# Optimization experiments

Hardware: AMD Instinct MI355X
Metric: run time of the kernel (lower is better)

## Reference

```python
import jax, jax.numpy as jnp
import numpy as np
from jax import lax

NUM_TAGS = 19
IN_DIM = 202
HID = 100
B, T = 256, 512


def setup_inputs() -> dict:
    key = jax.random.key(0)
    ks = jax.random.split(key, 16)
    u = lambda k, shape, s: jax.random.uniform(k, shape, jnp.float32, -s, s)
    sh = 1.0 / np.sqrt(HID)
    sl = 1.0 / np.sqrt(2 * HID)
    x = jax.random.normal(ks[0], (B, T, IN_DIM), jnp.float32)
    lengths = jax.random.randint(ks[1], (B,), 1, T + 1)
    raw_tags = jax.random.randint(ks[2], (B, T), 0, NUM_TAGS)
    y = jnp.where(jnp.arange(T)[None, :] < lengths[:, None], raw_tags, -1)
    return dict(
        x=x, y=y,
        w_ih_f=u(ks[3], (HID, IN_DIM), sh), w_hh_f=u(ks[4], (HID, HID), sh),
        b_ih_f=u(ks[5], (HID,), sh), b_hh_f=u(ks[6], (HID,), sh),
        w_ih_b=u(ks[7], (HID, IN_DIM), sh), w_hh_b=u(ks[8], (HID, HID), sh),
        b_ih_b=u(ks[9], (HID,), sh), b_hh_b=u(ks[10], (HID,), sh),
        w_lin=u(ks[11], (NUM_TAGS, 2 * HID), sl), b_lin=u(ks[12], (NUM_TAGS,), sl),
        start_trans=u(ks[13], (NUM_TAGS,), 0.1),
        end_trans=u(ks[14], (NUM_TAGS,), 0.1),
        trans=u(ks[15], (NUM_TAGS, NUM_TAGS), 0.1),
    )


def _rnn_dir(x, w_ih, w_hh, b_ih, b_hh, reverse):
    # torch nn.RNN (tanh) scans over axis 0 of x (batch_first=False semantics)
    def step(h, xt):
        h = jnp.tanh(xt @ w_ih.T + b_ih + h @ w_hh.T + b_hh)
        return h, h
    h0 = jnp.zeros((x.shape[1], w_hh.shape[0]), x.dtype)
    _, hs = lax.scan(step, h0, x, reverse=reverse)
    return hs  # (S, N, HID)


def _emissions(x, w_ih_f, w_hh_f, b_ih_f, b_hh_f, w_ih_b, w_hh_b, b_ih_b, b_hh_b, w_lin, b_lin):
    hf = _rnn_dir(x, w_ih_f, w_hh_f, b_ih_f, b_hh_f, False)
    hb = _rnn_dir(x, w_ih_b, w_hh_b, b_ih_b, b_hh_b, True)
    h = jnp.concatenate([hf, hb], axis=-1)  # (B, T, 200)
    return jax.nn.softmax(h @ w_lin.T + b_lin, axis=2)  # (B, T, 19)


def _crf_llh(em, tags, mask, start, end, trans):
    # emissions (B,T,K) batch_first -> transpose to (T,B,*) for the scans
    em_t = jnp.swapaxes(em, 0, 1)
    tg = jnp.where(jnp.swapaxes(mask, 0, 1), jnp.swapaxes(tags, 0, 1), 0)
    mk = jnp.swapaxes(mask, 0, 1)
    mf = mk.astype(em.dtype)
    # numerator: gold path score
    s0 = start[tg[0]] + jnp.take_along_axis(em_t[0], tg[0][:, None], 1)[:, 0]
    def num_step(carry, inp):
        s, prev = carry
        e, t, m, mb = inp
        emit = jnp.take_along_axis(e, t[:, None], 1)[:, 0]
        s = s + (trans[prev, t] + emit) * m
        prev = jnp.where(mb, t, prev)  # track tag at last valid position
        return (s, prev), None
    (num, last), _ = lax.scan(num_step, (s0, tg[0]), (em_t[1:], tg[1:], mf[1:], mk[1:]))
    num = num + end[last]
    # denominator: masked forward algorithm
    def z_step(s, inp):
        e, mb = inp
        nxt = jax.nn.logsumexp(s[:, :, None] + trans[None] + e[:, None, :], axis=1)
        return jnp.where(mb[:, None], nxt, s), None
    z, _ = lax.scan(z_step, start + em_t[0], (em_t[1:], mk[1:]))
    logz = jax.nn.logsumexp(z + end, axis=1)
    return num - logz  # (B,) log-likelihood per sequence


def _viterbi(em, mask, start, end, trans):
    em_t = jnp.swapaxes(em, 0, 1)
    mk = jnp.swapaxes(mask, 0, 1)
    def fstep(s, inp):
        e, mb = inp
        cand = s[:, :, None] + trans[None] + e[:, None, :]  # (B,K,K)
        nxt = jnp.where(mb[:, None], jnp.max(cand, axis=1), s)
        return nxt, jnp.argmax(cand, axis=1)
    score, hist = lax.scan(fstep, start + em_t[0], (em_t[1:], mk[1:]))  # hist (T-1,B,K)
    best_last = jnp.argmax(score + end, axis=1)  # tag at each sequence end
    def bstep(tag, inp):
        h, mb = inp
        prev = jnp.take_along_axis(h, tag[:, None], 1)[:, 0]
        tag = jnp.where(mb, prev, tag)
        return tag, tag
    _, tags_bt = lax.scan(bstep, best_last, (hist, mk[1:]), reverse=True)  # (T-1,B), position order
    tags = jnp.concatenate([tags_bt, best_last[None]], axis=0)  # (T,B)
    tags = jnp.swapaxes(tags, 0, 1)
    return jnp.where(mask, tags, -1)  # pad with -1 like the torch pad_sequence


def reference(x, y, w_ih_f, w_hh_f, b_ih_f, b_hh_f, w_ih_b, w_hh_b, b_ih_b, b_hh_b, w_lin, b_lin, start_trans, end_trans, trans):
    mask = y != -1
    em = _emissions(x, w_ih_f, w_hh_f, b_ih_f, b_hh_f, w_ih_b, w_hh_b, b_ih_b, b_hh_b, w_lin, b_lin)
    loss = -jnp.sum(_crf_llh(em, y, mask, start_trans, end_trans, trans))  # reduction='sum'
    label = _viterbi(em, mask, start_trans, end_trans, trans)
    return loss, label
```

## Files before the change

kernel.cpp:

```cpp
#include <hip/hip_runtime.h>
#include <hip/hip_bf16.h>

#define B_ 256
#define T_ 512
#define IN_ 202
#define HID_ 100
#define K_ 19

typedef __attribute__((ext_vector_type(8))) short short8v;
typedef __attribute__((ext_vector_type(4))) float f32x4;

__device__ __forceinline__ float rl_f(float v, int l) {
  return __int_as_float(__builtin_amdgcn_readlane(__float_as_int(v), l));
}

__global__ __launch_bounds__(256, 1) void k_wprep(
    const float* __restrict__ wf, const float* __restrict__ wb,
    unsigned short* __restrict__ w3) {
  int idx = blockIdx.x * 256 + threadIdx.x;
  if (idx >= 224 * 224) return;
  int c = idx / 224, k = idx - (idx / 224) * 224;
  float v = 0.f;
  if (k < IN_) {
    if (c < 100) v = wf[c * IN_ + k];
    else if (c < 200) v = wb[(c - 100) * IN_ + k];
  }
  unsigned u0 = __float_as_uint(v) & 0xffff0000u;
  float r1 = v - __uint_as_float(u0);
  unsigned u1 = __float_as_uint(r1) & 0xffff0000u;
  float r2 = r1 - __uint_as_float(u1);
  w3[idx] = (unsigned short)(u0 >> 16);
  w3[50176 + idx] = (unsigned short)(u1 >> 16);
  w3[100352 + idx] = (unsigned short)(__float_as_uint(r2) >> 16);
}

__global__ __launch_bounds__(256, 2) void k_ih(
    const float* __restrict__ x, const unsigned short* __restrict__ w3,
    const float* __restrict__ bif, const float* __restrict__ bhf,
    const float* __restrict__ bib, const float* __restrict__ bhb,
    float* __restrict__ pre) {
  __shared__ float xs[256 * 36];
  __shared__ float bsum[224];
  int tid = threadIdx.x;
  int wv = tid >> 6, l = tid & 63;
  long row0 = (long)blockIdx.x * 256;
  for (int u = tid; u < 224; u += 256) {
    float bv = 0.f;
    if (u < 100) bv = bif[u] + bhf[u];
    else if (u < 200) bv = bib[u - 100] + bhb[u - 100];
    bsum[u] = bv;
  }
  int lr = l & 15;
  int kq = l >> 4;
  for (int g = 0; g < 2; g++) {
    f32x4 acc[4][7];
#pragma unroll
    for (int m = 0; m < 4; m++)
#pragma unroll
      for (int n = 0; n < 7; n++) acc[m][n] = (f32x4){0.f, 0.f, 0.f, 0.f};
    for (int ck = 0; ck < 7; ck++) {
      int k0 = ck * 32;
      __syncthreads();
#pragma unroll
      for (int i = 0; i < 16; i++) {
        int u = tid + i * 256;
        int r = u >> 4, kp = u & 15;
        int gk = k0 + 2 * kp;
        float2 v = make_float2(0.f, 0.f);
        if (gk < IN_) v = *(const float2*)(x + (row0 + r) * IN_ + gk);
        *(float2*)(&xs[r * 36 + 2 * kp]) = v;
      }
      __syncthreads();
      short8v A0[4], A1[4], A2[4];
#pragma unroll
      for (int m = 0; m < 4; m++) {
        const float* ap = &xs[(wv * 64 + m * 16 + lr) * 36 + kq * 8];
        float4 fa = *(const float4*)(ap);
        float4 fb = *(const float4*)(ap + 4);
        float f[8] = {fa.x, fa.y, fa.z, fa.w, fb.x, fb.y, fb.z, fb.w};
#pragma unroll
        for (int j = 0; j < 8; j++) {
          unsigned u0 = __float_as_uint(f[j]) & 0xffff0000u;
          float r1 = f[j] - __uint_as_float(u0);
          unsigned u1 = __float_as_uint(r1) & 0xffff0000u;
          float r2 = r1 - __uint_as_float(u1);
          A0[m][j] = (short)(u0 >> 16);
          A1[m][j] = (short)(u1 >> 16);
          A2[m][j] = (short)(__float_as_uint(r2) >> 16);
        }
      }
#pragma unroll
      for (int n = 0; n < 7; n++) {
        int col = (g * 7 + n) * 16 + lr;
        const unsigned short* bp = w3 + (long)col * 224 + k0 + kq * 8;
        short8v B0 = *(const short8v*)(bp);
        short8v B1 = *(const short8v*)(bp + 50176);
        short8v B2 = *(const short8v*)(bp + 100352);
#pragma unroll
        for (int m = 0; m < 4; m++) {
          f32x4 c = acc[m][n];
          c = __builtin_amdgcn_mfma_f32_16x16x32_bf16(A0[m], B0, c, 0, 0, 0);
          c = __builtin_amdgcn_mfma_f32_16x16x32_bf16(A0[m], B1, c, 0, 0, 0);
          c = __builtin_amdgcn_mfma_f32_16x16x32_bf16(A1[m], B0, c, 0, 0, 0);
          c = __builtin_amdgcn_mfma_f32_16x16x32_bf16(A0[m], B2, c, 0, 0, 0);
          c = __builtin_amdgcn_mfma_f32_16x16x32_bf16(A2[m], B0, c, 0, 0, 0);
          c = __builtin_amdgcn_mfma_f32_16x16x32_bf16(A1[m], B1, c, 0, 0, 0);
          c = __builtin_amdgcn_mfma_f32_16x16x32_bf16(A1[m], B2, c, 0, 0, 0);
          c = __builtin_amdgcn_mfma_f32_16x16x32_bf16(A2[m], B1, c, 0, 0, 0);
          acc[m][n] = c;
        }
      }
    }
#pragma unroll
    for (int m = 0; m < 4; m++) {
      long rbase = row0 + wv * 64 + m * 16 + kq * 4;
#pragma unroll
      for (int n = 0; n < 7; n++) {
        int col = (g * 7 + n) * 16 + lr;
        if (col < 200) {
          float bv = bsum[col];
#pragma unroll
          for (int r = 0; r < 4; r++)
            pre[(rbase + r) * 200 + col] = acc[m][n][r] + bv;
        }
      }
    }
  }
}

template <int KO, int KN, bool OW>
__device__ __forceinline__ void rnn_loop(
    float* __restrict__ p, long step, int row, bool owns,
    const float* __restrict__ w, float (*hb)[104], float* __restrict__ ps) {
  float wr[KN];
#pragma unroll
  for (int i = 0; i < KN / 4; i++) {
    float4 w4 = *(const float4*)(w + row * HID_ + KO + 4 * i);
    wr[4 * i + 0] = w4.x; wr[4 * i + 1] = w4.y;
    wr[4 * i + 2] = w4.z; wr[4 * i + 3] = w4.w;
  }
  float a = 0.f;
  if (OW) a = p[row];
  for (int s = 0; s < B_; s++) {
    int cur = s & 1;
    float a_next = 0.f;
    if (OW && s < B_ - 1) a_next = p[step + row];
    float ac0 = OW ? a : 0.f, ac1 = 0.f, ac2 = 0.f, ac3 = 0.f;
#pragma unroll
    for (int i = 0; i < KN / 4; i++) {
      float4 h4 = *(const float4*)(&hb[cur][KO + 4 * i]);
      ac0 = fmaf(h4.x, wr[4 * i + 0], ac0);
      ac1 = fmaf(h4.y, wr[4 * i + 1], ac1);
      ac2 = fmaf(h4.z, wr[4 * i + 2], ac2);
      ac3 = fmaf(h4.w, wr[4 * i + 3], ac3);
    }
    float partial = (ac0 + ac1) + (ac2 + ac3);
    if (!OW && owns) ps[row] = partial;
    __syncthreads();
    if (OW) {
      float hnew = tanhf(partial + ps[row]);
      if (owns) {
        hb[cur ^ 1][row] = hnew;
        p[row] = hnew;
      }
    }
    p += step;
    a = a_next;
    __syncthreads();
  }
}

__global__ __launch_bounds__(256, 4) void k_rnn(
    float* __restrict__ pre,
    const float* __restrict__ whf, const float* __restrict__ whb) {
  __shared__ float hb[2][104];
  __shared__ float ps[104];
  int bid = blockIdx.x;
  int dir = bid >> 9;
  int t = bid & 511;
  const float* w = dir ? whb : whf;
  int tid = threadIdx.x;
  int wv = tid >> 6, lane = tid & 63;
  int grp = wv >> 1;
  int khalf = wv & 1;
  int row = grp ? (64 + (lane < 36 ? lane : 35)) : lane;
  bool owns = grp ? (lane < 36) : true;
  long step = dir ? -(long)(T_ * 200) : (long)(T_ * 200);
  float* p = pre + ((long)(dir ? (B_ - 1) : 0) * T_ + t) * 200 + dir * 100;
  if (tid < 104) hb[0][tid] = 0.f;
  __syncthreads();
  if (khalf == 0) rnn_loop<0, 52, true >(p, step, row, owns, w, hb, ps);
  else            rnn_loop<52, 48, false>(p, step, row, owns, w, hb, ps);
}

__global__ __launch_bounds__(256, 4) void k_lin(
    const float* __restrict__ h, const float* __restrict__ wlin,
    const float* __restrict__ blin, float* __restrict__ em) {
  int tid = threadIdx.x;
  long r0 = ((long)blockIdx.x * 256 + tid) * 2;
  const float* h0 = h + r0 * 200;
  float acc0[K_], acc1[K_];
#pragma unroll
  for (int c = 0; c < K_; c++) { float bb = blin[c]; acc0[c] = bb; acc1[c] = bb; }
  for (int kk = 0; kk < 50; kk++) {
    float4 a = *(const float4*)(h0 + 4 * kk);
    float4 b = *(const float4*)(h0 + 200 + 4 * kk);
#pragma unroll
    for (int c = 0; c < K_; c++) {
      float4 wv = *(const float4*)(wlin + c * 200 + 4 * kk);
      acc0[c] += a.x * wv.x + a.y * wv.y + a.z * wv.z + a.w * wv.w;
      acc1[c] += b.x * wv.x + b.y * wv.y + b.z * wv.z + b.w * wv.w;
    }
  }
  float mx0 = acc0[0], mx1 = acc1[0];
#pragma unroll
  for (int c = 1; c < K_; c++) { mx0 = fmaxf(mx0, acc0[c]); mx1 = fmaxf(mx1, acc1[c]); }
  float s0 = 0.f, s1 = 0.f;
#pragma unroll
  for (int c = 0; c < K_; c++) {
    acc0[c] = __expf(acc0[c] - mx0); s0 += acc0[c];
    acc1[c] = __expf(acc1[c] - mx1); s1 += acc1[c];
  }
  float i0 = 1.f / s0, i1 = 1.f / s1;
  float* e0 = em + r0 * K_;
#pragma unroll
  for (int c = 0; c < K_; c++) { e0[c] = acc0[c] * i0; e0[K_ + c] = acc1[c] * i1; }
}

__global__ __launch_bounds__(128, 1) void k_crf(
    const float* __restrict__ em, const int* __restrict__ y,
    const float* __restrict__ st_g, const float* __restrict__ en_g,
    const float* __restrict__ tr_g,
    float* __restrict__ part, int* __restrict__ cnt,
    float* __restrict__ out) {
  __shared__ __align__(16) float es[T_ * K_];
  __shared__ int ys[T_];
  __shared__ float tr[K_ * K_];
  __shared__ float st[K_], en[K_];
  __shared__ unsigned char hl[511 * K_ + 13];
  __shared__ float lab[T_];
  int b = blockIdx.x;
  int tid = threadIdx.x;
  const float4* eb4 = (const float4*)(em + (long)b * T_ * K_);
  for (int u = tid; u < T_ * K_ / 4; u += 128) ((float4*)es)[u] = eb4[u];
  for (int u = tid; u < T_; u += 128) ys[u] = y[b * T_ + u];
  for (int u = tid; u < K_ * K_; u += 128) tr[u] = tr_g[u];
  if (tid < K_) { st[tid] = st_g[tid]; en[tid] = en_g[tid]; }
  __syncthreads();
  int wv = tid >> 6, lane = tid & 63;
  int jj = lane < K_ ? lane : K_ - 1;
  bool act = lane < K_;
  if (wv == 0) {
    float E[K_];
#pragma unroll
    for (int i = 0; i < K_; i++) E[i] = __expf(tr[i * K_ + jj]);
    float z = act ? st[jj] + es[jj] : -1e30f;
    int y0 = ys[0];
    int prev = (y0 != -1) ? y0 : 0;
    float num = st[prev] + es[prev];
    for (int t = 1; t < T_; t++) {
      float e = es[t * K_ + jj];
      int yv = ys[t];
      bool mb = (yv != -1);
      float m = z;
#pragma unroll
      for (int off = 16; off; off >>= 1) m = fmaxf(m, __shfl_xor(m, off, 32));
      float pz = __expf(z - m);
      float acca = 0.f, accb = 0.f;
#pragma unroll
      for (int i = 0; i < 9; i++)  acca = fmaf(rl_f(pz, i), E[i], acca);
#pragma unroll
      for (int i = 9; i < K_; i++) accb = fmaf(rl_f(pz, i), E[i], accb);
      float nz = e + m + __logf(acca + accb);
      if (act && mb) z = nz;
      if (mb) {
        num += tr[prev * K_ + yv] + es[t * K_ + yv];
        prev = yv;
      }
    }
    num += en[prev];
    float zf = z + en[jj];
    float m2 = zf;
#pragma unroll
    for (int off = 16; off; off >>= 1) m2 = fmaxf(m2, __shfl_xor(m2, off, 32));
    float sm = __expf(zf - m2);
#pragma unroll
    for (int off = 16; off; off >>= 1) sm += __shfl_xor(sm, off, 32);
    if (lane == 0) part[b] = m2 + __logf(sm) - num;
  } else {
    float Tt[K_];
#pragma unroll
    for (int i = 0; i < K_; i++) Tt[i] = tr[i * K_ + jj];
    float v = act ? st[jj] + es[jj] : -1e30f;
    for (int t = 1; t < T_; t++) {
      float e = es[t * K_ + jj];
      int yv = ys[t];
      bool mb = (yv != -1);
      float b0 = -1e30f, b1 = -1e30f, b2 = -1e30f, b3 = -1e30f;
      int a0 = 0, a1 = 5, a2 = 10, a3 = 15;
#pragma unroll
      for (int i = 0; i < 5; i++)  { float c = rl_f(v, i) + Tt[i]; if (c > b0) { b0 = c; a0 = i; } }
#pragma unroll
      for (int i = 5; i < 10; i++) { float c = rl_f(v, i) + Tt[i]; if (c > b1) { b1 = c; a1 = i; } }
#pragma unroll
      for (int i = 10; i < 15; i++){ float c = rl_f(v, i) + Tt[i]; if (c > b2) { b2 = c; a2 = i; } }
#pragma unroll
      for (int i = 15; i < 19; i++){ float c = rl_f(v, i) + Tt[i]; if (c > b3) { b3 = c; a3 = i; } }
      if (b1 > b0) { b0 = b1; a0 = a1; }
      if (b2 > b0) { b0 = b2; a0 = a2; }
      if (b3 > b0) { b0 = b3; a0 = a3; }
      if (act) hl[(t - 1) * K_ + lane] = (unsigned char)a0;
      if (act && mb) v = b0 + e;
    }
    float sc = v + en[jj];
    float bb = -1e30f; int aa = 0;
#pragma unroll
    for (int i = 0; i < K_; i++) { float c = rl_f(sc, i); if (c > bb) { bb = c; aa = i; } }
    int tag = aa;
    if (lane == 0) lab[T_ - 1] = (ys[T_ - 1] != -1) ? (float)tag : -1.f;
    int vc = (lane < K_) ? (int)hl[510 * K_ + lane] : 0;
    for (int ti = 510; ti >= 0; ti--) {
      int vn = 0;
      if (ti > 0 && lane < K_) vn = (int)hl[(ti - 1) * K_ + lane];
      int ts = __builtin_amdgcn_readfirstlane(tag);
      int cand = __builtin_amdgcn_readlane(vc, ts);
      tag = (ys[ti + 1] != -1) ? cand : tag;
      if (lane == 0) lab[ti] = (ys[ti] != -1) ? (float)tag : -1.f;
      vc = vn;
    }
  }
  __syncthreads();
  if (wv == 1) {
    float* ob = out + 1 + (long)b * T_;
    for (int u = lane; u < T_; u += 64) ob[u] = lab[u];
  } else {
    int old = -1;
    if (lane == 0) { __threadfence(); old = atomicAdd(cnt, 1); }
    old = __shfl(old, 0, 64);
    if (old == B_ - 1) {
      __threadfence();
      float s = 0.f;
      for (int u = lane; u < B_; u += 64) s += part[u];
#pragma unroll
      for (int off = 32; off; off >>= 1) s += __shfl_xor(s, off, 64);
      if (lane == 0) out[0] = s;
    }
  }
}

extern "C" void kernel_launch(void* const* d_in, const int* in_sizes, int n_in,
                              void* d_out, int out_size, void* d_ws, size_t ws_size,
                              hipStream_t stream) {
  const float* x      = (const float*)d_in[0];
  const int*   y      = (const int*)d_in[1];
  const float* w_ih_f = (const float*)d_in[2];
  const float* w_hh_f = (const float*)d_in[3];
  const float* b_ih_f = (const float*)d_in[4];
  const float* b_hh_f = (const float*)d_in[5];
  const float* w_ih_b = (const float*)d_in[6];
  const float* w_hh_b = (const float*)d_in[7];
  const float* b_ih_b = (const float*)d_in[8];
  const float* b_hh_b = (const float*)d_in[9];
  const float* w_lin  = (const float*)d_in[10];
  const float* b_lin  = (const float*)d_in[11];
  const float* st     = (const float*)d_in[12];
  const float* en     = (const float*)d_in[13];
  const float* trans  = (const float*)d_in[14];

  char* ws = (char*)d_ws;
  const size_t PRE_OFF  = 0;
  const size_t EM_OFF   = 104857600;
  const size_t PART_OFF = EM_OFF + 9961472;
  const size_t CNT_OFF  = PART_OFF + 1024;
  float* PRE  = (float*)(ws + PRE_OFF);
  float* EM   = (float*)(ws + EM_OFF);
  float* PART = (float*)(ws + PART_OFF);
  int*   CNT  = (int*)(ws + CNT_OFF);
  unsigned short* W3 = (unsigned short*)(ws + EM_OFF);
  float* out  = (float*)d_out;

  hipMemsetAsync((void*)CNT, 0, sizeof(int), stream);
  k_wprep<<<196, 256, 0, stream>>>(w_ih_f, w_ih_b, W3);
  k_ih<<<512, 256, 0, stream>>>(x, W3, b_ih_f, b_hh_f, b_ih_b, b_hh_b, PRE);
  k_rnn<<<1024, 256, 0, stream>>>(PRE, w_hh_f, w_hh_b);
  k_lin<<<256, 256, 0, stream>>>(PRE, w_lin, b_lin, EM);
  k_crf<<<256, 128, 0, stream>>>(EM, y, st, en, trans, PART, CNT, out);
}
```

Measured before the change: 666.1 us.

## Merge CRF forward and Viterbi into one wave, loop only to sequence length

The CRF kernel now runs the log-sum-exp forward recursion and the Viterbi max recursion in a single 64-lane wavefront instead of two waves. It computes each sequence's length from the mask and iterates only up to that length instead of all 512 steps, which removes the per-step mask checks. Padding labels are written directly, so the shared label buffer goes away. The forward pass now uses lane 0's value as the stabilizer instead of a max reduction. This relies on masks being contiguous prefixes and accepts some numerical risk from that stabilizer.

```diff
diff --git a/kernel.cpp b/kernel.cpp
--- a/kernel.cpp
+++ b/kernel.cpp
@@ -227,7 +227,7 @@
   for (int c = 0; c < K_; c++) { e0[c] = acc0[c] * i0; e0[K_ + c] = acc1[c] * i1; }
 }
 
-__global__ __launch_bounds__(128, 1) void k_crf(
+__global__ __launch_bounds__(64, 1) void k_crf(
     const float* __restrict__ em, const int* __restrict__ y,
     const float* __restrict__ st_g, const float* __restrict__ en_g,
     const float* __restrict__ tr_g,
@@ -235,116 +235,110 @@
     float* __restrict__ out) {
   __shared__ __align__(16) float es[T_ * K_];
   __shared__ int ys[T_];
-  __shared__ float tr[K_ * K_];
+  __shared__ float trs[K_ * K_];
   __shared__ float st[K_], en[K_];
   __shared__ unsigned char hl[511 * K_ + 13];
-  __shared__ float lab[T_];
   int b = blockIdx.x;
-  int tid = threadIdx.x;
+  int lane = threadIdx.x;
   const float4* eb4 = (const float4*)(em + (long)b * T_ * K_);
-  for (int u = tid; u < T_ * K_ / 4; u += 128) ((float4*)es)[u] = eb4[u];
-  for (int u = tid; u < T_; u += 128) ys[u] = y[b * T_ + u];
-  for (int u = tid; u < K_ * K_; u += 128) tr[u] = tr_g[u];
-  if (tid < K_) { st[tid] = st_g[tid]; en[tid] = en_g[tid]; }
+  for (int u = lane; u < T_ * K_ / 4; u += 64) ((float4*)es)[u] = eb4[u];
+  for (int u = lane; u < T_; u += 64) ys[u] = y[b * T_ + u];
+  for (int u = lane; u < K_ * K_; u += 64) trs[u] = tr_g[u];
+  if (lane < K_) { st[lane] = st_g[lane]; en[lane] = en_g[lane]; }
   __syncthreads();
-  int wv = tid >> 6, lane = tid & 63;
+  int lmin = T_;
+  for (int u = lane; u < T_; u += 64)
+    if (ys[u] == -1 && u < lmin) lmin = u;
+#pragma unroll
+  for (int off = 32; off; off >>= 1) {
+    int o = __shfl_xor(lmin, off, 64);
+    lmin = lmin < o ? lmin : o;
+  }
+  int len = lmin;
+
   int jj = lane < K_ ? lane : K_ - 1;
   bool act = lane < K_;
-  if (wv == 0) {
-    float E[K_];
-#pragma unroll
-    for (int i = 0; i < K_; i++) E[i] = __expf(tr[i * K_ + jj]);
-    float z = act ? st[jj] + es[jj] : -1e30f;
-    int y0 = ys[0];
-    int prev = (y0 != -1) ? y0 : 0;
-    float num = st[prev] + es[prev];
-    for (int t = 1; t < T_; t++) {
-      float e = es[t * K_ + jj];
-      int yv = ys[t];
-      bool mb = (yv != -1);
-      float m = z;
-#pragma unroll
-      for (int off = 16; off; off >>= 1) m = fmaxf(m, __shfl_xor(m, off, 32));
-      float pz = __expf(z - m);
-      float acca = 0.f, accb = 0.f;
-#pragma unroll
-      for (int i = 0; i < 9; i++)  acca = fmaf(rl_f(pz, i), E[i], acca);
-#pragma unroll
-      for (int i = 9; i < K_; i++) accb = fmaf(rl_f(pz, i), E[i], accb);
-      float nz = e + m + __logf(acca + accb);
-      if (act && mb) z = nz;
-      if (mb) {
-        num += tr[prev * K_ + yv] + es[t * K_ + yv];
-        prev = yv;
-      }
-    }
-    num += en[prev];
-    float zf = z + en[jj];
-    float m2 = zf;
-#pragma unroll
-    for (int off = 16; off; off >>= 1) m2 = fmaxf(m2, __shfl_xor(m2, off, 32));
-    float sm = __expf(zf - m2);
-#pragma unroll
-    for (int off = 16; off; off >>= 1) sm += __shfl_xor(sm, off, 32);
-    if (lane == 0) part[b] = m2 + __logf(sm) - num;
-  } else {
-    float Tt[K_];
-#pragma unroll
-    for (int i = 0; i < K_; i++) Tt[i] = tr[i * K_ + jj];
-    float v = act ? st[jj] + es[jj] : -1e30f;
-    for (int t = 1; t < T_; t++) {
-      float e = es[t * K_ + jj];
-      int yv = ys[t];
-      bool mb = (yv != -1);
-      float b0 = -1e30f, b1 = -1e30f, b2 = -1e30f, b3 = -1e30f;
-      int a0 = 0, a1 = 5, a2 = 10, a3 = 15;
-#pragma unroll
-      for (int i = 0; i < 5; i++)  { float c = rl_f(v, i) + Tt[i]; if (c > b0) { b0 = c; a0 = i; } }
-#pragma unroll
-      for (int i = 5; i < 10; i++) { float c = rl_f(v, i) + Tt[i]; if (c > b1) { b1 = c; a1 = i; } }
-#pragma unroll
-      for (int i = 10; i < 15; i++){ float c = rl_f(v, i) + Tt[i]; if (c > b2) { b2 = c; a2 = i; } }
-#pragma unroll
-      for (int i = 15; i < 19; i++){ float c = rl_f(v, i) + Tt[i]; if (c > b3) { b3 = c; a3 = i; } }
-      if (b1 > b0) { b0 = b1; a0 = a1; }
-      if (b2 > b0) { b0 = b2; a0 = a2; }
-      if (b3 > b0) { b0 = b3; a0 = a3; }
-      if (act) hl[(t - 1) * K_ + lane] = (unsigned char)a0;
-      if (act && mb) v = b0 + e;
-    }
-    float sc = v + en[jj];
-    float bb = -1e30f; int aa = 0;
-#pragma unroll
-    for (int i = 0; i < K_; i++) { float c = rl_f(sc, i); if (c > bb) { bb = c; aa = i; } }
-    int tag = aa;
-    if (lane == 0) lab[T_ - 1] = (ys[T_ - 1] != -1) ? (float)tag : -1.f;
-    int vc = (lane < K_) ? (int)hl[510 * K_ + lane] : 0;
-    for (int ti = 510; ti >= 0; ti--) {
-      int vn = 0;
-      if (ti > 0 && lane < K_) vn = (int)hl[(ti - 1) * K_ + lane];
-      int ts = __builtin_amdgcn_readfirstlane(tag);
-      int cand = __builtin_amdgcn_readlane(vc, ts);
-      tag = (ys[ti + 1] != -1) ? cand : tag;
-      if (lane == 0) lab[ti] = (ys[ti] != -1) ? (float)tag : -1.f;
-      vc = vn;
-    }
-  }
-  __syncthreads();
-  if (wv == 1) {
-    float* ob = out + 1 + (long)b * T_;
-    for (int u = lane; u < T_; u += 64) ob[u] = lab[u];
-  } else {
-    int old = -1;
-    if (lane == 0) { __threadfence(); old = atomicAdd(cnt, 1); }
-    old = __shfl(old, 0, 64);
-    if (old == B_ - 1) {
-      __threadfence();
-      float s = 0.f;
-      for (int u = lane; u < B_; u += 64) s += part[u];
-#pragma unroll
-      for (int off = 32; off; off >>= 1) s += __shfl_xor(s, off, 64);
-      if (lane == 0) out[0] = s;
-    }
+  float E[K_], Tt[K_];
+#pragma unroll
+  for (int i = 0; i < K_; i++) {
+    float tv = trs[i * K_ + jj];
+    E[i] = __expf(tv);
+    Tt[i] = tv;
+  }
+  float z = act ? st[jj] + es[jj] : -1e30f;
+  float v = z;
+  int prev = ys[0];
+  float num = st[prev] + es[prev];
+  float e = es[K_ + jj];
+  for (int t = 1; t < len; t++) {
+    int tn = t + 1 < T_ ? t + 1 : T_ - 1;
+    float e_next = es[tn * K_ + jj];
+    int yv = ys[t];
+    float s = rl_f(z, 0);
+    float pz = __expf(z - s);
+    float acca = 0.f, accb = 0.f;
+#pragma unroll
+    for (int i = 0; i < 9; i++)  acca = fmaf(rl_f(pz, i), E[i], acca);
+#pragma unroll
+    for (int i = 9; i < K_; i++) accb = fmaf(rl_f(pz, i), E[i], accb);
+    float nz = e + s + __logf(acca + accb);
+    num += trs[prev * K_ + yv] + rl_f(e, yv);
+    prev = yv;
+    float b0 = -1e30f, b1 = -1e30f, b2 = -1e30f, b3 = -1e30f;
+    int a0 = 0, a1 = 5, a2 = 10, a3 = 15;
+#pragma unroll
+    for (int i = 0; i < 5; i++)  { float c = rl_f(v, i) + Tt[i]; if (c > b0) { b0 = c; a0 = i; } }
+#pragma unroll
+    for (int i = 5; i < 10; i++) { float c = rl_f(v, i) + Tt[i]; if (c > b1) { b1 = c; a1 = i; } }
+#pragma unroll
+    for (int i = 10; i < 15; i++){ float c = rl_f(v, i) + Tt[i]; if (c > b2) { b2 = c; a2 = i; } }
+#pragma unroll
+    for (int i = 15; i < 19; i++){ float c = rl_f(v, i) + Tt[i]; if (c > b3) { b3 = c; a3 = i; } }
+    if (b1 > b0) { b0 = b1; a0 = a1; }
+    if (b2 > b0) { b0 = b2; a0 = a2; }
+    if (b3 > b0) { b0 = b3; a0 = a3; }
+    if (act) hl[(t - 1) * K_ + lane] = (unsigned char)a0;
+    z = act ? nz : z;
+    v = act ? b0 + e : v;
+    e = e_next;
+  }
+  num += en[prev];
+  float zf = act ? z + en[jj] : -1e30f;
+  float m2 = zf;
+#pragma unroll
+  for (int off = 16; off; off >>= 1) m2 = fmaxf(m2, __shfl_xor(m2, off, 32));
+  float sm = __expf(zf - m2);
+#pragma unroll
+  for (int off = 16; off; off >>= 1) sm += __shfl_xor(sm, off, 32);
+  if (lane == 0) part[b] = m2 + __logf(sm) - num;
+  float sc = act ? v + en[jj] : -1e30f;
+  float bb = -1e30f; int aa = 0;
+#pragma unroll
+  for (int i = 0; i < K_; i++) { float c = rl_f(sc, i); if (c > bb) { bb = c; aa = i; } }
+  float* ob = out + 1 + (long)b * T_;
+  for (int u = lane; u < T_; u += 64)
+    if (u >= len) ob[u] = -1.f;
+  int tag = aa;
+  if (lane == 0) ob[len - 1] = (float)tag;
+  int vc = (act && len >= 2) ? (int)hl[(len - 2) * K_ + lane] : 0;
+  for (int ti = len - 2; ti >= 0; ti--) {
+    int vn = 0;
+    if (ti > 0 && act) vn = (int)hl[(ti - 1) * K_ + lane];
+    int ts = __builtin_amdgcn_readfirstlane(tag);
+    tag = __builtin_amdgcn_readlane(vc, ts);
+    if (lane == 0) ob[ti] = (float)tag;
+    vc = vn;
+  }
+  int old = -1;
+  if (lane == 0) { __threadfence(); old = atomicAdd(cnt, 1); }
+  old = __shfl(old, 0, 64);
+  if (old == B_ - 1) {
+    __threadfence();
+    float s = 0.f;
+    for (int u = lane; u < B_; u += 64) s += part[u];
+#pragma unroll
+    for (int off = 32; off; off >>= 1) s += __shfl_xor(s, off, 64);
+    if (lane == 0) out[0] = s;
   }
 }
 
@@ -384,5 +378,5 @@
   k_ih<<<512, 256, 0, stream>>>(x, W3, b_ih_f, b_hh_f, b_ih_b, b_hh_b, PRE);
   k_rnn<<<1024, 256, 0, stream>>>(PRE, w_hh_f, w_hh_b);
   k_lin<<<256, 256, 0, stream>>>(PRE, w_lin, b_lin, EM);
-  k_crf<<<256, 128, 0, stream>>>(EM, y, st, en, trans, PART, CNT, out);
-}
+  k_crf<<<256, 64, 0, stream>>>(EM, y, st, en, trans, PART, CNT, out);
+}
```

Measured after the change: 703.9 us. 5.7% more time.
